# Kernel optimization log

Hardware: AMD Instinct MI355X
Metric: run time of the kernel (lower is better)

Reference implementation:

```python
import jax, jax.numpy as jnp
import numpy as np

D_MODEL = 1024
NUM_HEADS = 16
D_HEAD = D_MODEL // NUM_HEADS
ROPE_BASE = 10000.0


def _rope(x):
    # x: (B, H, S, Dh); lucidrains interleaved rotary along seq dim
    dh = x.shape[-1]
    s = x.shape[-2]
    inv_freq = 1.0 / (ROPE_BASE ** (jnp.arange(0, dh, 2, dtype=jnp.float32) / dh))
    freqs = jnp.arange(s, dtype=jnp.float32)[:, None] * inv_freq[None, :]  # (S, Dh/2)
    cos = jnp.repeat(jnp.cos(freqs), 2, axis=-1)  # (S, Dh), [f0,f0,f1,f1,...]
    sin = jnp.repeat(jnp.sin(freqs), 2, axis=-1)
    x1 = x[..., ::2]
    x2 = x[..., 1::2]
    rot = jnp.stack([-x2, x1], axis=-1).reshape(x.shape)  # rotate_half, interleaved
    return x * cos + rot * sin


def setup_inputs() -> dict:
    key = jax.random.key(0)
    ks = jax.random.split(key, 16)
    B, S, D, H, Dh = 8, 1024, D_MODEL, NUM_HEADS, D_HEAD
    scale = 1.0 / np.sqrt(D)
    inp = {
        "query": jax.random.normal(ks[0], (B, S, D), jnp.float32),
        "key": jax.random.normal(ks[1], (B, S, D), jnp.float32),
        "value": jax.random.normal(ks[2], (B, S, D), jnp.float32),
        "mask": jax.random.randint(ks[3], (B, S, S), 0, 2).astype(bool),
        "Wq": jax.random.normal(ks[4], (D, D), jnp.float32) * scale,
        "bq": jnp.zeros((D,), jnp.float32),
        "Wk": jax.random.normal(ks[5], (D, D), jnp.float32) * scale,
        "bk": jnp.zeros((D,), jnp.float32),
        "Wv": jax.random.normal(ks[6], (D, D), jnp.float32) * scale,
        "bv": jnp.zeros((D,), jnp.float32),
        "u_bias": jax.random.normal(ks[7], (H, Dh), jnp.float32) * (1.0 / np.sqrt(Dh)),
        "Wo": jax.random.normal(ks[8], (D, D), jnp.float32) * scale,
        "bo": jnp.zeros((D,), jnp.float32),
    }
    return inp


def reference(query, key, value, mask, Wq, bq, Wk, bk, Wv, bv, u_bias, Wo, bo):
    B, S, D = query.shape
    H, Dh = NUM_HEADS, D_HEAD
    # projections -> (B, H, S, Dh)
    q = (query @ Wq.T + bq).reshape(B, S, H, Dh).transpose(0, 2, 1, 3)
    k = (key @ Wk.T + bk).reshape(B, S, H, Dh).transpose(0, 2, 1, 3)
    v = (value @ Wv.T + bv).reshape(B, S, H, Dh).transpose(0, 2, 1, 3)
    q = _rope(q)  # (B, H, S, Dh)
    k = _rope(k)
    # (q + u_bias) @ k^T ; u_bias broadcasts over (H, Dh)
    qb = q + u_bias[None, :, None, :]
    score = jnp.einsum("bhsd,bhtd->bhst", qb, k) / np.sqrt(Dh)
    score = jnp.where(mask[:, None, :, :], -1e9, score)
    attn = jax.nn.softmax(score, axis=-1)  # dropout is identity in eval mode
    ctx = jnp.einsum("bhst,bhtd->bhsd", attn, v)  # (B, H, S, Dh)
    ctx = ctx.transpose(0, 2, 1, 3).reshape(B, S, D)
    return ctx @ Wo.T + bo
```

## Files before the change

kernel.cpp:

```cpp
#include <hip/hip_runtime.h>

#define S_LEN 1024
#define D_MODELX 1024
#define NHEAD 16
#define DHEAD 64
#define BATCH 8
#define NTOK (BATCH * S_LEN)
#define KSCALE 0.18033688011112f

typedef __bf16 bf16;
typedef __attribute__((ext_vector_type(8))) __bf16 bf16x8;
typedef __attribute__((ext_vector_type(4))) __bf16 bf16x4;
typedef __attribute__((ext_vector_type(4))) float f32x4;

__device__ __forceinline__ void gload_lds16(const void* gsrc, void* ldst) {
  __builtin_amdgcn_global_load_lds(
      (const __attribute__((address_space(1))) void*)gsrc,
      (__attribute__((address_space(3))) void*)ldst,
      16, 0, 0);
}

#define PRE_ACT_BLKS 8192
#define PRE_W_BLKS 1024
#define PRE_MASK_BLKS 32768
#define PRE_TOTAL (3 * PRE_ACT_BLKS + 4 * PRE_W_BLKS + PRE_MASK_BLKS + 128)
__global__ __launch_bounds__(256) void preproc(
    const float* __restrict__ q, const float* __restrict__ k,
    const float* __restrict__ v, const float* __restrict__ Wq,
    const float* __restrict__ Wk, const float* __restrict__ Wv,
    const float* __restrict__ Wo, const int* __restrict__ mask,
    bf16* __restrict__ Xq, bf16* __restrict__ Xk, bf16* __restrict__ Xv,
    bf16* __restrict__ Wqb, bf16* __restrict__ Wkb, bf16* __restrict__ Wvb,
    bf16* __restrict__ Wob, unsigned long long* __restrict__ mp,
    float* __restrict__ cosT, float* __restrict__ sinT) {
  int blk = blockIdx.x;
  int tid = threadIdx.x;
  if (blk < 3 * PRE_ACT_BLKS + 4 * PRE_W_BLKS) {
    const float* src;
    bf16* dst;
    int l;
    if (blk < PRE_ACT_BLKS) { src = q; dst = Xq; l = blk; }
    else if (blk < 2 * PRE_ACT_BLKS) { src = k; dst = Xk; l = blk - PRE_ACT_BLKS; }
    else if (blk < 3 * PRE_ACT_BLKS) { src = v; dst = Xv; l = blk - 2 * PRE_ACT_BLKS; }
    else if (blk < 3 * PRE_ACT_BLKS + PRE_W_BLKS) { src = Wq; dst = Wqb; l = blk - 3 * PRE_ACT_BLKS; }
    else if (blk < 3 * PRE_ACT_BLKS + 2 * PRE_W_BLKS) { src = Wk; dst = Wkb; l = blk - 3 * PRE_ACT_BLKS - PRE_W_BLKS; }
    else if (blk < 3 * PRE_ACT_BLKS + 3 * PRE_W_BLKS) { src = Wv; dst = Wvb; l = blk - 3 * PRE_ACT_BLKS - 2 * PRE_W_BLKS; }
    else { src = Wo; dst = Wob; l = blk - 3 * PRE_ACT_BLKS - 3 * PRE_W_BLKS; }
    int i = l * 256 + tid;
    float4 val = ((const float4*)src)[i];
    bf16x4 o;
    o[0] = (bf16)val.x; o[1] = (bf16)val.y; o[2] = (bf16)val.z; o[3] = (bf16)val.w;
    ((bf16x4*)dst)[i] = o;
  } else if (blk < 3 * PRE_ACT_BLKS + 4 * PRE_W_BLKS + PRE_MASK_BLKS) {
    int l = blk - (3 * PRE_ACT_BLKS + 4 * PRE_W_BLKS);
    int i = l * 256 + tid;
    unsigned long long bal = __ballot(mask[i] != 0);
    if ((tid & 63) == 0) mp[i >> 6] = bal;
  } else {
    int l = blk - (3 * PRE_ACT_BLKS + 4 * PRE_W_BLKS + PRE_MASK_BLKS);
    int idx = l * 256 + tid;
    int s = idx >> 5;
    int i = idx & 31;
    float inv = powf(10000.0f, -(float)i / 32.0f);
    float f = (float)s * inv;
    cosT[idx] = cosf(f);
    sinT[idx] = sinf(f);
  }
}

template <int MODE>
__global__ __launch_bounds__(256) void gemm_bt(
    const bf16* __restrict__ X, const bf16* __restrict__ W,
    const float* __restrict__ bias, void* __restrict__ outp,
    const float* __restrict__ cosT, const float* __restrict__ sinT,
    const float* __restrict__ ubias) {
  __shared__ bf16 At[128 * 32];
  __shared__ bf16 Bt[128 * 32];
  const int id = blockIdx.x;
  const int swz = (id & 7) * 64 + (id >> 3);
  const int m0 = (swz >> 3) * 128;
  const int n0 = (swz & 7) * 128;
  const int tid = threadIdx.x;
  const int lane = tid & 63;
  const int wid = tid >> 6;
  const int g = lane >> 4;
  const int li = lane & 15;
  const int wr = (wid >> 1) * 64;
  const int wc = (wid & 1) * 64;

  f32x4 acc[4][4] = {};

  for (int k0 = 0; k0 < D_MODELX; k0 += 32) {
    __syncthreads();
#pragma unroll
    for (int c = 0; c < 2; ++c) {
      int chunk = wid * 128 + c * 64 + lane;
      int r = chunk >> 2;
      int seg = chunk & 3;
      gload_lds16(X + (size_t)(m0 + r) * D_MODELX + k0 + seg * 8,
                  &At[(wid * 128 + c * 64) * 8]);
      gload_lds16(W + (size_t)(n0 + r) * D_MODELX + k0 + seg * 8,
                  &Bt[(wid * 128 + c * 64) * 8]);
    }
    __syncthreads();
    bf16x8 af[4], bfr[4];
#pragma unroll
    for (int m = 0; m < 4; ++m)
      af[m] = *(const bf16x8*)&At[(wr + m * 16 + li) * 32 + g * 8];
#pragma unroll
    for (int n = 0; n < 4; ++n)
      bfr[n] = *(const bf16x8*)&Bt[(wc + n * 16 + li) * 32 + g * 8];
#pragma unroll
    for (int m = 0; m < 4; ++m)
#pragma unroll
      for (int n = 0; n < 4; ++n)
        acc[m][n] = __builtin_amdgcn_mfma_f32_16x16x32_bf16(af[m], bfr[n],
                                                            acc[m][n], 0, 0, 0);
  }

#pragma unroll
  for (int m = 0; m < 4; ++m) {
#pragma unroll
    for (int n = 0; n < 4; ++n) {
      int col = n0 + wc + n * 16 + li;
      if (MODE == 2) {
        int token0 = m0 + wr + m * 16 + g * 4;
        int s0 = token0 & (S_LEN - 1);
        int b0 = token0 >> 10;
        int dh = col & 63;
        int h = col >> 6;
        bf16x4 o;
#pragma unroll
        for (int rg = 0; rg < 4; ++rg) o[rg] = (bf16)(acc[m][n][rg] + bias[col]);
        *(bf16x4*)&((bf16*)outp)[(((size_t)b0 * NHEAD + h) * DHEAD + dh) * S_LEN + s0] = o;
      } else {
#pragma unroll
        for (int rg = 0; rg < 4; ++rg) {
          int token = m0 + wr + m * 16 + g * 4 + rg;
          float v = acc[m][n][rg] + bias[col];
          if (MODE <= 1) {
            float p = __shfl_xor(v, 1, 64);
            int s = token & (S_LEN - 1);
            int b = token >> 10;
            int dh = col & 63;
            int h = col >> 6;
            int fi = dh >> 1;
            float cv = cosT[s * 32 + fi];
            float sv = sinT[s * 32 + fi];
            float vr = (dh & 1) ? (v * cv + p * sv) : (v * cv - p * sv);
            if (MODE == 0) vr += ubias[(h << 6) + dh];
            if (MODE == 1) vr *= KSCALE;
            ((bf16*)outp)[(((size_t)b * NHEAD + h) * S_LEN + s) * DHEAD + dh] = (bf16)vr;
          } else {
            ((float*)outp)[(size_t)token * D_MODELX + col] = v;
          }
        }
      }
    }
  }
}

__global__ __launch_bounds__(256) void attn_fwd(
    const bf16* __restrict__ Q, const bf16* __restrict__ K,
    const bf16* __restrict__ V, const unsigned long long* __restrict__ mp,
    bf16* __restrict__ ctx) {
  __shared__ bf16 Kl[2][64 * 64];
  __shared__ bf16 Vt[2][64 * 64];
  __shared__ bf16 Pl[4][16 * 64];

  const int id = blockIdx.x;
  const int swz = (id & 7) * 256 + (id >> 3);
  const int bh = swz >> 4;
  const int qblk = swz & 15;
  const int tid = threadIdx.x;
  const int lane = tid & 63;
  const int wid = tid >> 6;
  const int b = bh >> 4;
  const int h = bh & 15;
  const int g = lane >> 4;
  const int li = lane & 15;
  const int q0 = qblk * 64 + wid * 16;

  const bf16* qbase = Q + ((size_t)bh * S_LEN + q0) * DHEAD;
  bf16x8 qf[2];
  qf[0] = *(const bf16x8*)&qbase[(size_t)li * DHEAD + g * 8];
  qf[1] = *(const bf16x8*)&qbase[(size_t)li * DHEAD + 32 + g * 8];

  bf16x8 onesf;
#pragma unroll
  for (int j = 0; j < 8; ++j) onesf[j] = (bf16)1.0f;

  f32x4 ctxacc[4] = {};
  f32x4 sacc = {};

  const bf16* gk = K + (size_t)bh * S_LEN * DHEAD;
  const bf16* gv = V + (size_t)bh * DHEAD * S_LEN;
  const unsigned long long* mrowp = mp + ((size_t)b * S_LEN + q0) * 16;

  const int srow = lane >> 3;
  const int schunk = (lane & 7) ^ srow;

  auto stage = [&](int bi, int it) {
    int t0 = it * 64;
#pragma unroll
    for (int j = 0; j < 2; ++j) {
      int row = wid * 16 + j * 8 + srow;
      gload_lds16(gk + ((size_t)(t0 + row)) * DHEAD + schunk * 8,
                  &Kl[bi][(wid * 16 + j * 8) * 64]);
      gload_lds16(gv + (size_t)row * S_LEN + t0 + schunk * 8,
                  &Vt[bi][(wid * 16 + j * 8) * 64]);
    }
  };

  stage(0, 0);
  int buf = 0;

  for (int it = 0; it < S_LEN / 64; ++it) {
    asm volatile("s_waitcnt vmcnt(0)" ::: "memory");
    __builtin_amdgcn_s_barrier();
    if (it + 1 < S_LEN / 64) stage(buf ^ 1, it + 1);

    unsigned long long mw[4];
#pragma unroll
    for (int rg = 0; rg < 4; ++rg)
      mw[rg] = mrowp[(size_t)(g * 4 + rg) * 16 + it];

    f32x4 sc[4];
#pragma unroll
    for (int tt = 0; tt < 4; ++tt) {
      int row = tt * 16 + li;
      int sz = li & 7;
      bf16x8 kf0 = *(const bf16x8*)&Kl[buf][row * 64 + ((g ^ sz) << 3)];
      bf16x8 kf1 = *(const bf16x8*)&Kl[buf][row * 64 + (((g + 4) ^ sz) << 3)];
      f32x4 a = {};
      a = __builtin_amdgcn_mfma_f32_16x16x32_bf16(qf[0], kf0, a, 0, 0, 0);
      a = __builtin_amdgcn_mfma_f32_16x16x32_bf16(qf[1], kf1, a, 0, 0, 0);
      sc[tt] = a;
    }

#pragma unroll
    for (int rg = 0; rg < 4; ++rg) {
      unsigned long long msh = mw[rg] >> li;
      unsigned int mlo = (unsigned int)msh;
      unsigned int mhi = (unsigned int)(msh >> 32);
      int qq = g * 4 + rg;
#pragma unroll
      for (int tt = 0; tt < 4; ++tt) {
        unsigned int half = (tt & 2) ? mhi : mlo;
        unsigned int bit = (half >> ((tt & 1) << 4)) & 1u;
        float p = exp2f(sc[tt][rg]);
        p = bit ? 0.0f : p;
        int t = tt * 16 + li;
        Pl[wid][qq * 64 + (t ^ ((qq & 7) << 3))] = (bf16)p;
      }
    }

#pragma unroll
    for (int sub = 0; sub < 2; ++sub) {
      bf16x8 pf = *(const bf16x8*)&Pl[wid][li * 64 + (((sub * 4 + g) ^ (li & 7)) << 3)];
      sacc = __builtin_amdgcn_mfma_f32_16x16x32_bf16(pf, onesf, sacc, 0, 0, 0);
#pragma unroll
      for (int dd = 0; dd < 4; ++dd) {
        int row = dd * 16 + li;
        bf16x8 vf = *(const bf16x8*)&Vt[buf][row * 64 + (((sub * 4 + g) ^ (row & 7)) << 3)];
        ctxacc[dd] = __builtin_amdgcn_mfma_f32_16x16x32_bf16(pf, vf, ctxacc[dd], 0, 0, 0);
      }
    }
    buf ^= 1;
  }

  float inv[4];
#pragma unroll
  for (int rg = 0; rg < 4; ++rg) inv[rg] = 1.0f / sacc[rg];
#pragma unroll
  for (int dd = 0; dd < 4; ++dd)
#pragma unroll
    for (int rg = 0; rg < 4; ++rg) {
      float vout = ctxacc[dd][rg] * inv[rg];
      int s = q0 + g * 4 + rg;
      int d = h * 64 + dd * 16 + li;
      ctx[((size_t)b * S_LEN + s) * D_MODELX + d] = (bf16)vout;
    }
}

extern "C" void kernel_launch(void* const* d_in, const int* in_sizes, int n_in,
                              void* d_out, int out_size, void* d_ws, size_t ws_size,
                              hipStream_t stream) {
  const float* query = (const float*)d_in[0];
  const float* key   = (const float*)d_in[1];
  const float* value = (const float*)d_in[2];
  const int*   mask  = (const int*)d_in[3];
  const float* Wq = (const float*)d_in[4];
  const float* bq = (const float*)d_in[5];
  const float* Wk = (const float*)d_in[6];
  const float* bk = (const float*)d_in[7];
  const float* Wv = (const float*)d_in[8];
  const float* bv = (const float*)d_in[9];
  const float* ub = (const float*)d_in[10];
  const float* Wo = (const float*)d_in[11];
  const float* bo = (const float*)d_in[12];
  float* out = (float*)d_out;

  char* wsb = (char*)d_ws;
  size_t off = 0;
  auto give = [&](size_t bytes) -> char* {
    char* p = wsb + off;
    off += (bytes + 255) & ~(size_t)255;
    return p;
  };
  const size_t ACT = (size_t)NTOK * D_MODELX * 2;
  const size_t WB  = (size_t)D_MODELX * D_MODELX * 2;
  bf16* Xq   = (bf16*)give(ACT);
  bf16* Xk   = (bf16*)give(ACT);
  bf16* Xv   = (bf16*)give(ACT);
  bf16* Wqb  = (bf16*)give(WB);
  bf16* Wkb  = (bf16*)give(WB);
  bf16* Wvb  = (bf16*)give(WB);
  bf16* Wob  = (bf16*)give(WB);
  bf16* qws  = (bf16*)give(ACT);
  bf16* kws  = (bf16*)give(ACT);
  bf16* vws  = (bf16*)give(ACT);
  unsigned long long* mp = (unsigned long long*)give((size_t)BATCH * S_LEN * 16 * 8);
  float* cosT = (float*)give((size_t)S_LEN * 32 * 4);
  float* sinT = (float*)give((size_t)S_LEN * 32 * 4);
  bf16* ctxw = Xq;

  preproc<<<PRE_TOTAL, 256, 0, stream>>>(query, key, value, Wq, Wk, Wv, Wo, mask,
                                         Xq, Xk, Xv, Wqb, Wkb, Wvb, Wob, mp,
                                         cosT, sinT);

  gemm_bt<0><<<512, 256, 0, stream>>>(Xq, Wqb, bq, qws, cosT, sinT, ub);
  gemm_bt<1><<<512, 256, 0, stream>>>(Xk, Wkb, bk, kws, cosT, sinT, ub);
  gemm_bt<2><<<512, 256, 0, stream>>>(Xv, Wvb, bv, vws, cosT, sinT, ub);

  attn_fwd<<<2048, 256, 0, stream>>>(qws, kws, vws, mp, ctxw);

  gemm_bt<3><<<512, 256, 0, stream>>>(ctxw, Wob, bo, out, cosT, sinT, ub);
}
```

Before: 380.8 us.

## Fuse QKV projections into one GEMM launch, widen K tile, prioritize attention MFMAs

```diff
diff --git a/kernel.cpp b/kernel.cpp
--- a/kernel.cpp
+++ b/kernel.cpp
@@ -68,14 +68,113 @@
   }
 }
 
-template <int MODE>
-__global__ __launch_bounds__(256) void gemm_bt(
-    const bf16* __restrict__ X, const bf16* __restrict__ W,
-    const float* __restrict__ bias, void* __restrict__ outp,
+__global__ __launch_bounds__(256) void gemm_qkv(
+    const bf16* __restrict__ Xq, const bf16* __restrict__ Xk,
+    const bf16* __restrict__ Xv, const bf16* __restrict__ W3,
+    const float* __restrict__ bq, const float* __restrict__ bk,
+    const float* __restrict__ bv,
+    bf16* __restrict__ qws, bf16* __restrict__ kws, bf16* __restrict__ vws,
     const float* __restrict__ cosT, const float* __restrict__ sinT,
     const float* __restrict__ ubias) {
-  __shared__ bf16 At[128 * 32];
-  __shared__ bf16 Bt[128 * 32];
+  __shared__ bf16 At[128 * 64];
+  __shared__ bf16 Bt[128 * 64];
+  const int id = blockIdx.x;
+  const int xcd = id & 7;
+  const int idx = id >> 3;
+  const int mpan = xcd * 8 + idx / 24;
+  const int nblk = idx % 24;
+  const int m0 = mpan * 128;
+  const int n0 = nblk * 128;
+  const int proj = nblk >> 3;
+  const bf16* X = proj == 0 ? Xq : proj == 1 ? Xk : Xv;
+  const float* bias = proj == 0 ? bq : proj == 1 ? bk : bv;
+
+  const int tid = threadIdx.x;
+  const int lane = tid & 63;
+  const int wid = tid >> 6;
+  const int g = lane >> 4;
+  const int li = lane & 15;
+  const int wr = (wid >> 1) * 64;
+  const int wc = (wid & 1) * 64;
+
+  f32x4 acc[4][4] = {};
+
+  for (int k0 = 0; k0 < D_MODELX; k0 += 64) {
+    __syncthreads();
+#pragma unroll
+    for (int c = 0; c < 4; ++c) {
+      int chunk = (c * 4 + wid) * 64 + lane;
+      int r = chunk >> 3;
+      int seg = chunk & 7;
+      gload_lds16(X + (size_t)(m0 + r) * D_MODELX + k0 + seg * 8,
+                  &At[((c * 4 + wid) * 64) * 8]);
+      gload_lds16(W3 + (size_t)(n0 + r) * D_MODELX + k0 + seg * 8,
+                  &Bt[((c * 4 + wid) * 64) * 8]);
+    }
+    __syncthreads();
+#pragma unroll
+    for (int kk = 0; kk < 2; ++kk) {
+      bf16x8 af[4], bfr[4];
+#pragma unroll
+      for (int m = 0; m < 4; ++m)
+        af[m] = *(const bf16x8*)&At[(wr + m * 16 + li) * 64 + kk * 32 + g * 8];
+#pragma unroll
+      for (int n = 0; n < 4; ++n)
+        bfr[n] = *(const bf16x8*)&Bt[(wc + n * 16 + li) * 64 + kk * 32 + g * 8];
+#pragma unroll
+      for (int m = 0; m < 4; ++m)
+#pragma unroll
+        for (int n = 0; n < 4; ++n)
+          acc[m][n] = __builtin_amdgcn_mfma_f32_16x16x32_bf16(af[m], bfr[n],
+                                                              acc[m][n], 0, 0, 0);
+    }
+  }
+
+#pragma unroll
+  for (int m = 0; m < 4; ++m) {
+#pragma unroll
+    for (int n = 0; n < 4; ++n) {
+      int col = n0 + wc + n * 16 + li;
+      int col1k = col & 1023;
+      int dh = col1k & 63;
+      int h = col1k >> 6;
+      if (proj == 2) {
+        int token0 = m0 + wr + m * 16 + g * 4;
+        int s0 = token0 & (S_LEN - 1);
+        int b0 = token0 >> 10;
+        bf16x4 o;
+#pragma unroll
+        for (int rg = 0; rg < 4; ++rg) o[rg] = (bf16)(acc[m][n][rg] + bias[col1k]);
+        *(bf16x4*)&vws[(((size_t)b0 * NHEAD + h) * DHEAD + dh) * S_LEN + s0] = o;
+      } else {
+#pragma unroll
+        for (int rg = 0; rg < 4; ++rg) {
+          int token = m0 + wr + m * 16 + g * 4 + rg;
+          float v = acc[m][n][rg] + bias[col1k];
+          float p = __shfl_xor(v, 1, 64);
+          int s = token & (S_LEN - 1);
+          int b = token >> 10;
+          int fi = dh >> 1;
+          float cv = cosT[s * 32 + fi];
+          float sv = sinT[s * 32 + fi];
+          float vr = (dh & 1) ? (v * cv + p * sv) : (v * cv - p * sv);
+          if (proj == 0) {
+            vr += ubias[(h << 6) + dh];
+            qws[(((size_t)b * NHEAD + h) * S_LEN + s) * DHEAD + dh] = (bf16)vr;
+          } else {
+            kws[(((size_t)b * NHEAD + h) * S_LEN + s) * DHEAD + dh] = (bf16)(vr * KSCALE);
+          }
+        }
+      }
+    }
+  }
+}
+
+__global__ __launch_bounds__(256) void gemm_out(
+    const bf16* __restrict__ X, const bf16* __restrict__ W,
+    const float* __restrict__ bias, float* __restrict__ outp) {
+  __shared__ bf16 At[128 * 64];
+  __shared__ bf16 Bt[128 * 64];
   const int id = blockIdx.x;
   const int swz = (id & 7) * 64 + (id >> 3);
   const int m0 = (swz >> 3) * 128;
@@ -90,74 +189,48 @@
 
   f32x4 acc[4][4] = {};
 
-  for (int k0 = 0; k0 < D_MODELX; k0 += 32) {
+  for (int k0 = 0; k0 < D_MODELX; k0 += 64) {
     __syncthreads();
 #pragma unroll
-    for (int c = 0; c < 2; ++c) {
-      int chunk = wid * 128 + c * 64 + lane;
-      int r = chunk >> 2;
-      int seg = chunk & 3;
+    for (int c = 0; c < 4; ++c) {
+      int chunk = (c * 4 + wid) * 64 + lane;
+      int r = chunk >> 3;
+      int seg = chunk & 7;
       gload_lds16(X + (size_t)(m0 + r) * D_MODELX + k0 + seg * 8,
-                  &At[(wid * 128 + c * 64) * 8]);
+                  &At[((c * 4 + wid) * 64) * 8]);
       gload_lds16(W + (size_t)(n0 + r) * D_MODELX + k0 + seg * 8,
-                  &Bt[(wid * 128 + c * 64) * 8]);
+                  &Bt[((c * 4 + wid) * 64) * 8]);
     }
     __syncthreads();
-    bf16x8 af[4], bfr[4];
-#pragma unroll
-    for (int m = 0; m < 4; ++m)
-      af[m] = *(const bf16x8*)&At[(wr + m * 16 + li) * 32 + g * 8];
-#pragma unroll
-    for (int n = 0; n < 4; ++n)
-      bfr[n] = *(const bf16x8*)&Bt[(wc + n * 16 + li) * 32 + g * 8];
-#pragma unroll
-    for (int m = 0; m < 4; ++m)
+#pragma unroll
+    for (int kk = 0; kk < 2; ++kk) {
+      bf16x8 af[4], bfr[4];
+#pragma unroll
+      for (int m = 0; m < 4; ++m)
+        af[m] = *(const bf16x8*)&At[(wr + m * 16 + li) * 64 + kk * 32 + g * 8];
 #pragma unroll
       for (int n = 0; n < 4; ++n)
-        acc[m][n] = __builtin_amdgcn_mfma_f32_16x16x32_bf16(af[m], bfr[n],
-                                                            acc[m][n], 0, 0, 0);
+        bfr[n] = *(const bf16x8*)&Bt[(wc + n * 16 + li) * 64 + kk * 32 + g * 8];
+#pragma unroll
+      for (int m = 0; m < 4; ++m)
+#pragma unroll
+        for (int n = 0; n < 4; ++n)
+          acc[m][n] = __builtin_amdgcn_mfma_f32_16x16x32_bf16(af[m], bfr[n],
+                                                              acc[m][n], 0, 0, 0);
+    }
   }
 
 #pragma unroll
-  for (int m = 0; m < 4; ++m) {
+  for (int m = 0; m < 4; ++m)
 #pragma unroll
     for (int n = 0; n < 4; ++n) {
       int col = n0 + wc + n * 16 + li;
-      if (MODE == 2) {
-        int token0 = m0 + wr + m * 16 + g * 4;
-        int s0 = token0 & (S_LEN - 1);
-        int b0 = token0 >> 10;
-        int dh = col & 63;
-        int h = col >> 6;
-        bf16x4 o;
-#pragma unroll
-        for (int rg = 0; rg < 4; ++rg) o[rg] = (bf16)(acc[m][n][rg] + bias[col]);
-        *(bf16x4*)&((bf16*)outp)[(((size_t)b0 * NHEAD + h) * DHEAD + dh) * S_LEN + s0] = o;
-      } else {
-#pragma unroll
-        for (int rg = 0; rg < 4; ++rg) {
-          int token = m0 + wr + m * 16 + g * 4 + rg;
-          float v = acc[m][n][rg] + bias[col];
-          if (MODE <= 1) {
-            float p = __shfl_xor(v, 1, 64);
-            int s = token & (S_LEN - 1);
-            int b = token >> 10;
-            int dh = col & 63;
-            int h = col >> 6;
-            int fi = dh >> 1;
-            float cv = cosT[s * 32 + fi];
-            float sv = sinT[s * 32 + fi];
-            float vr = (dh & 1) ? (v * cv + p * sv) : (v * cv - p * sv);
-            if (MODE == 0) vr += ubias[(h << 6) + dh];
-            if (MODE == 1) vr *= KSCALE;
-            ((bf16*)outp)[(((size_t)b * NHEAD + h) * S_LEN + s) * DHEAD + dh] = (bf16)vr;
-          } else {
-            ((float*)outp)[(size_t)token * D_MODELX + col] = v;
-          }
-        }
+#pragma unroll
+      for (int rg = 0; rg < 4; ++rg) {
+        int token = m0 + wr + m * 16 + g * 4 + rg;
+        outp[(size_t)token * D_MODELX + col] = acc[m][n][rg] + bias[col];
       }
     }
-  }
 }
 
 __global__ __launch_bounds__(256) void attn_fwd(
@@ -226,6 +299,7 @@
       mw[rg] = mrowp[(size_t)(g * 4 + rg) * 16 + it];
 
     f32x4 sc[4];
+    __builtin_amdgcn_s_setprio(1);
 #pragma unroll
     for (int tt = 0; tt < 4; ++tt) {
       int row = tt * 16 + li;
@@ -237,6 +311,7 @@
       a = __builtin_amdgcn_mfma_f32_16x16x32_bf16(qf[1], kf1, a, 0, 0, 0);
       sc[tt] = a;
     }
+    __builtin_amdgcn_s_setprio(0);
 
 #pragma unroll
     for (int rg = 0; rg < 4; ++rg) {
@@ -255,6 +330,7 @@
       }
     }
 
+    __builtin_amdgcn_s_setprio(1);
 #pragma unroll
     for (int sub = 0; sub < 2; ++sub) {
       bf16x8 pf = *(const bf16x8*)&Pl[wid][li * 64 + (((sub * 4 + g) ^ (li & 7)) << 3)];
@@ -266,6 +342,7 @@
         ctxacc[dd] = __builtin_amdgcn_mfma_f32_16x16x32_bf16(pf, vf, ctxacc[dd], 0, 0, 0);
       }
     }
+    __builtin_amdgcn_s_setprio(0);
     buf ^= 1;
   }
 
@@ -329,11 +406,10 @@
                                          Xq, Xk, Xv, Wqb, Wkb, Wvb, Wob, mp,
                                          cosT, sinT);
 
-  gemm_bt<0><<<512, 256, 0, stream>>>(Xq, Wqb, bq, qws, cosT, sinT, ub);
-  gemm_bt<1><<<512, 256, 0, stream>>>(Xk, Wkb, bk, kws, cosT, sinT, ub);
-  gemm_bt<2><<<512, 256, 0, stream>>>(Xv, Wvb, bv, vws, cosT, sinT, ub);
+  gemm_qkv<<<1536, 256, 0, stream>>>(Xq, Xk, Xv, Wqb, bq, bk, bv,
+                                     qws, kws, vws, cosT, sinT, ub);
 
   attn_fwd<<<2048, 256, 0, stream>>>(qws, kws, vws, mp, ctxw);
 
-  gemm_bt<3><<<512, 256, 0, stream>>>(ctxw, Wob, bo, out, cosT, sinT, ub);
-}
+  gemm_out<<<512, 256, 0, stream>>>(ctxw, Wob, bo, out);
+}
```

Result: slower. 418.8 us (+10.0%).
